# Kernel optimization log

Measured on AMD Instinct MI355X. Metric: run time of the kernel, lower is better.

## Reference

```python
import jax, jax.numpy as jnp
import numpy as np

D_MODEL = 1024
N_HEADS = 16
HEAD = D_MODEL // N_HEADS  # 64


def setup_inputs() -> dict:
    key = jax.random.key(0)
    ks = jax.random.split(key, 9)
    s = 1.0 / np.sqrt(D_MODEL)
    x = jax.random.normal(ks[0], (2, 2048, D_MODEL), dtype=jnp.float32)
    Wq = jax.random.uniform(ks[1], (N_HEADS, D_MODEL, HEAD), jnp.float32, -s, s)
    bq = jax.random.uniform(ks[2], (N_HEADS, HEAD), jnp.float32, -s, s)
    Wk = jax.random.uniform(ks[3], (N_HEADS, D_MODEL, HEAD), jnp.float32, -s, s)
    bk = jax.random.uniform(ks[4], (N_HEADS, HEAD), jnp.float32, -s, s)
    Wv = jax.random.uniform(ks[5], (N_HEADS, D_MODEL, HEAD), jnp.float32, -s, s)
    bv = jax.random.uniform(ks[6], (N_HEADS, HEAD), jnp.float32, -s, s)
    Wo = jax.random.uniform(ks[7], (D_MODEL, D_MODEL), jnp.float32, -s, s)
    bo = jax.random.uniform(ks[8], (D_MODEL,), jnp.float32, -s, s)
    return {"x": x, "Wq": Wq, "bq": bq, "Wk": Wk, "bk": bk,
            "Wv": Wv, "bv": bv, "Wo": Wo, "bo": bo}


def reference(x, Wq, bq, Wk, bk, Wv, bv, Wo, bo):
    # Per-head projections, vectorized over heads: [B,S,D] x [H,D,h] -> [B,H,S,h]
    Q = jnp.einsum('bsd,hdk->bhsk', x, Wq) + bq[None, :, None, :]
    K = jnp.einsum('bsd,hdk->bhsk', x, Wk) + bk[None, :, None, :]
    V = jnp.einsum('bsd,hdk->bhsk', x, Wv) + bv[None, :, None, :]
    scores = jnp.einsum('bhqk,bhsk->bhqs', Q, K) / jnp.sqrt(jnp.float32(HEAD))
    attn = jax.nn.softmax(scores, axis=-1)  # dropout is identity in eval mode
    out = jnp.einsum('bhqs,bhsk->bhqk', attn, V)  # [B,H,S,h]
    B, H, S, h = out.shape
    out = out.transpose(0, 2, 1, 3).reshape(B, S, H * h)  # concat heads -> [B,S,D]
    return out @ Wo.T + bo if False else jnp.einsum('bsd,ed->bse', out, Wo.T.T) + bo
```

## Files before the change

kernel.cpp:

```cpp
#include <hip/hip_runtime.h>
#include <hip/hip_bf16.h>

typedef unsigned short u16;
typedef short short8 __attribute__((ext_vector_type(8)));
typedef float floatx4 __attribute__((ext_vector_type(4)));

#define MFMA16(a, b, c) __builtin_amdgcn_mfma_f32_16x16x32_bf16((a), (b), (c), 0, 0, 0)

union U64u { unsigned long long ll; u16 s[4]; };
union U128u { uint4 q; u16 s[8]; };

__device__ __forceinline__ u16 f2bf(float f) {
  union { float f; unsigned u; } v; v.f = f;
  unsigned r = v.u + 0x7fffu + ((v.u >> 16) & 1u);
  return (u16)(r >> 16);
}

__device__ __forceinline__ void async16(const u16* g, u16* l) {
  __builtin_amdgcn_global_load_lds(
      (const __attribute__((address_space(1))) unsigned int*)g,
      (__attribute__((address_space(3))) unsigned int*)l, 16, 0, 0);
}


__global__ __launch_bounds__(256) void cast_f2b(const float* __restrict__ src,
                                                u16* __restrict__ dst, int n4) {
  int i = blockIdx.x * 256 + threadIdx.x;
  if (i >= n4) return;
  float4 v = ((const float4*)src)[i];
  U64u o;
  o.s[0] = f2bf(v.x); o.s[1] = f2bf(v.y); o.s[2] = f2bf(v.z); o.s[3] = f2bf(v.w);
  ((unsigned long long*)dst)[i] = o.ll;
}

__global__ __launch_bounds__(256) void prep_wqkv(
    const float* __restrict__ Wq, const float* __restrict__ bq,
    const float* __restrict__ Wk, const float* __restrict__ bk,
    const float* __restrict__ Wv, const float* __restrict__ bv,
    u16* __restrict__ Wt, float* __restrict__ ball) {
  int id = blockIdx.x * 256 + threadIdx.x;
  int kk4 = id & 15;
  int d = (id >> 4) & 1023;
  int h = (id >> 14) & 15;
  int wsel = id >> 18;
  const float* W = wsel == 0 ? Wq : (wsel == 1 ? Wk : Wv);
  float4 v = *(const float4*)(W + ((size_t)(h * 1024 + d)) * 64 + kk4 * 4);
  int nb = wsel * 1024 + h * 64 + kk4 * 4;
  Wt[(size_t)(nb + 0) * 1024 + d] = f2bf(v.x);
  Wt[(size_t)(nb + 1) * 1024 + d] = f2bf(v.y);
  Wt[(size_t)(nb + 2) * 1024 + d] = f2bf(v.z);
  Wt[(size_t)(nb + 3) * 1024 + d] = f2bf(v.w);
  if (id < 3072) {
    int ws2 = id >> 10, hk = id & 1023;
    const float* bsrc = ws2 == 0 ? bq : (ws2 == 1 ? bk : bv);
    ball[id] = bsrc[hk];
  }
}

__global__ __launch_bounds__(256) void transpose_v(const u16* __restrict__ QKV,
                                                   u16* __restrict__ Vt) {
  __shared__ u16 t[64][65];
  int tid = threadIdx.x;
  int bh = blockIdx.y, b = bh >> 4, h = bh & 15;
  int s0 = blockIdx.x * 64;
  {
    int r = tid >> 2, c0 = (tid & 3) * 16;
    const u16* src = QKV + (size_t)(b * 2048 + s0 + r) * 3072 + 2048 + h * 64 + c0;
    U128u a, c;
    a.q = *(const uint4*)src;
    c.q = *(const uint4*)(src + 8);
#pragma unroll
    for (int j = 0; j < 8; ++j) { t[r][c0 + j] = a.s[j]; t[r][c0 + 8 + j] = c.s[j]; }
  }
  __syncthreads();
  {
    int dl = tid >> 2, sp = (tid & 3) * 16;
    U128u oa, ob;
#pragma unroll
    for (int j = 0; j < 8; ++j) { oa.s[j] = t[sp + j][dl]; ob.s[j] = t[sp + 8 + j][dl]; }
    u16* dst = Vt + (size_t)(bh * 64 + dl) * 2048 + s0 + sp;
    *(uint4*)dst = oa.q;
    *(uint4*)(dst + 8) = ob.q;
  }
}


__device__ __forceinline__ void store_out(u16* p, float v) { *p = f2bf(v); }
__device__ __forceinline__ void store_out(float* p, float v) { *p = v; }

template <typename OutT>
__global__ __launch_bounds__(256) void gemm_bt(
    const u16* __restrict__ A, const u16* __restrict__ B,
    const float* __restrict__ bias, OutT* __restrict__ C,
    int M, int N, int K, int scaleNend, float scaleVal) {
  __shared__ __attribute__((aligned(16))) u16 As[128 * 32];
  __shared__ __attribute__((aligned(16))) u16 Bs[128 * 32];
  const int tid = threadIdx.x;
  const int w = tid >> 6, lane = tid & 63;
  const int l15 = lane & 15, l4 = lane >> 4;
  const int bm = blockIdx.y, bn = blockIdx.x;
  const int wm = (w & 1) * 64, wn = (w >> 1) * 64;

  floatx4 acc[4][4];
#pragma unroll
  for (int i = 0; i < 4; ++i)
#pragma unroll
    for (int j = 0; j < 4; ++j) acc[i][j] = (floatx4){0.f, 0.f, 0.f, 0.f};

  for (int k0 = 0; k0 < K; k0 += 32) {
    __syncthreads();
#pragma unroll
    for (int j = 0; j < 2; ++j) {
      int c = j * 4 + w;
      int row = c * 16 + (lane >> 2);
      int ko = (lane & 3) * 8;
      async16(A + (size_t)(bm * 128 + row) * K + k0 + ko, As + c * 512);
      async16(B + (size_t)(bn * 128 + row) * K + k0 + ko, Bs + c * 512);
    }
    __syncthreads();
    short8 af[4], bf[4];
#pragma unroll
    for (int t = 0; t < 4; ++t) {
      af[t] = *(const short8*)(As + (wm + t * 16 + l15) * 32 + l4 * 8);
      bf[t] = *(const short8*)(Bs + (wn + t * 16 + l15) * 32 + l4 * 8);
    }
#pragma unroll
    for (int tm = 0; tm < 4; ++tm)
#pragma unroll
      for (int tn = 0; tn < 4; ++tn) acc[tm][tn] = MFMA16(af[tm], bf[tn], acc[tm][tn]);
  }

#pragma unroll
  for (int tn = 0; tn < 4; ++tn) {
    int col = bn * 128 + wn + tn * 16 + l15;
    float bv = bias[col];
    float sc = (col < scaleNend) ? scaleVal : 1.0f;
#pragma unroll
    for (int tm = 0; tm < 4; ++tm) {
      int row0 = bm * 128 + wm + tm * 16 + l4 * 4;
#pragma unroll
      for (int r = 0; r < 4; ++r) {
        float v = (acc[tm][tn][r] + bv) * sc;
        store_out(C + (size_t)(row0 + r) * N + col, v);
      }
    }
  }
}


__global__ __launch_bounds__(256) void attn_kernel(const u16* __restrict__ QKV,
                                                   const u16* __restrict__ Vt,
                                                   u16* __restrict__ O) {
  __shared__ __attribute__((aligned(16))) u16 Ks[128 * 64];
  __shared__ __attribute__((aligned(16))) u16 Vs[64 * 128];
  __shared__ __attribute__((aligned(16))) u16 Ps[128 * 136];

  const int tid = threadIdx.x;
  const int w = tid >> 6, lane = tid & 63;
  const int l15 = lane & 15, l4 = lane >> 4;
  const int q0 = blockIdx.x * 128;
  const int bh = blockIdx.y;
  const int b = bh >> 4, h = bh & 15;

  short8 qf[2][2];
  {
    const u16* Qb = QKV + (size_t)(b * 2048 + q0 + w * 32) * 3072 + h * 64;
#pragma unroll
    for (int tq = 0; tq < 2; ++tq)
#pragma unroll
      for (int kc = 0; kc < 2; ++kc)
        qf[tq][kc] = *(const short8*)(Qb + (size_t)(tq * 16 + l15) * 3072 + kc * 32 + l4 * 8);
  }

  floatx4 Oacc[2][4];
#pragma unroll
  for (int i = 0; i < 2; ++i)
#pragma unroll
    for (int j = 0; j < 4; ++j) Oacc[i][j] = (floatx4){0.f, 0.f, 0.f, 0.f};
  float lpart[2] = {0.f, 0.f};

  const u16* Kb = QKV + (size_t)(b * 2048) * 3072 + 1024 + h * 64;
  const u16* Vb = Vt + (size_t)bh * 64 * 2048;

  for (int kt = 0; kt < 16; ++kt) {
    __syncthreads();
#pragma unroll
    for (int j = 0; j < 4; ++j) {
      int c = j * 4 + w;
      {
        int row = c * 8 + (lane >> 3);
        int gch = (lane & 7) ^ ((lane >> 3) & 7);
        async16(Kb + (size_t)(kt * 128 + row) * 3072 + gch * 8, Ks + c * 512);
      }
      {
        int d = c * 4 + l4;
        int gch = l15 ^ (d & 15);
        async16(Vb + (size_t)d * 2048 + kt * 128 + gch * 8, Vs + c * 512);
      }
    }
    __syncthreads();

#pragma unroll
    for (int tk = 0; tk < 8; ++tk) {
      int krow = tk * 16 + l15;
      int sw = krow & 7;
      short8 kf0 = *(const short8*)(Ks + krow * 64 + ((l4) ^ sw) * 8);
      short8 kf1 = *(const short8*)(Ks + krow * 64 + ((4 + l4) ^ sw) * 8);
#pragma unroll
      for (int tq = 0; tq < 2; ++tq) {
        floatx4 s = (floatx4){0.f, 0.f, 0.f, 0.f};
        s = MFMA16(kf0, qf[tq][0], s);
        s = MFMA16(kf1, qf[tq][1], s);
        U64u pk;
#pragma unroll
        for (int r = 0; r < 4; ++r) {
          float p = __expf(s[r]);
          lpart[tq] += p;
          pk.s[r] = f2bf(p);
        }
        *(unsigned long long*)(Ps + (size_t)(w * 32 + tq * 16 + l15) * 136 + tk * 16 + l4 * 4) = pk.ll;
      }
    }

    short8 pf[2][4];
#pragma unroll
    for (int tq = 0; tq < 2; ++tq)
#pragma unroll
      for (int kc = 0; kc < 4; ++kc)
        pf[tq][kc] = *(const short8*)(Ps + (size_t)(w * 32 + tq * 16 + l15) * 136 + kc * 32 + l4 * 8);
#pragma unroll
    for (int td = 0; td < 4; ++td)
#pragma unroll
      for (int kc = 0; kc < 4; ++kc) {
        int drow = td * 16 + l15;
        short8 vf = *(const short8*)(Vs + drow * 128 + (((kc << 2) | l4) ^ l15) * 8);
#pragma unroll
        for (int tq = 0; tq < 2; ++tq) Oacc[tq][td] = MFMA16(pf[tq][kc], vf, Oacc[tq][td]);
      }
  }

  float linv[2];
#pragma unroll
  for (int tq = 0; tq < 2; ++tq) {
    float l = lpart[tq];
    l += __shfl_xor(l, 16);
    l += __shfl_xor(l, 32);
    linv[tq] = 1.0f / l;
  }
  float iv[2][4];
#pragma unroll
  for (int tq = 0; tq < 2; ++tq)
#pragma unroll
    for (int r = 0; r < 4; ++r) iv[tq][r] = __shfl(linv[tq], l4 * 4 + r);

  u16* Ob = O + (size_t)(b * 2048 + q0 + w * 32) * 1024 + h * 64;
#pragma unroll
  for (int tq = 0; tq < 2; ++tq)
#pragma unroll
    for (int td = 0; td < 4; ++td)
#pragma unroll
      for (int r = 0; r < 4; ++r)
        Ob[(size_t)(tq * 16 + l4 * 4 + r) * 1024 + td * 16 + l15] =
            f2bf(Oacc[tq][td][r] * iv[tq][r]);
}


extern "C" void kernel_launch(void* const* d_in, const int* in_sizes, int n_in,
                              void* d_out, int out_size, void* d_ws, size_t ws_size,
                              hipStream_t stream) {
  const float* x  = (const float*)d_in[0];
  const float* Wq = (const float*)d_in[1];
  const float* bq = (const float*)d_in[2];
  const float* Wk = (const float*)d_in[3];
  const float* bk = (const float*)d_in[4];
  const float* Wv = (const float*)d_in[5];
  const float* bv = (const float*)d_in[6];
  const float* Wo = (const float*)d_in[7];
  const float* bo = (const float*)d_in[8];

  char* p = (char*)d_ws;
  u16* Xb   = (u16*)p; p += (size_t)4096 * 1024 * 2;
  u16* Wt   = (u16*)p; p += (size_t)3072 * 1024 * 2;
  u16* QKV  = (u16*)p; p += (size_t)4096 * 3072 * 2;
  u16* Vtp  = (u16*)p; p += (size_t)2 * 16 * 64 * 2048 * 2;
  u16* Ob   = (u16*)p; p += (size_t)4096 * 1024 * 2;
  u16* Wob  = (u16*)p; p += (size_t)1024 * 1024 * 2;
  float* ball = (float*)p; p += 3072 * sizeof(float);

  cast_f2b<<<4096, 256, 0, stream>>>(x, Xb, 1048576);
  cast_f2b<<<1024, 256, 0, stream>>>(Wo, Wob, 262144);
  prep_wqkv<<<3072, 256, 0, stream>>>(Wq, bq, Wk, bk, Wv, bv, Wt, ball);
  gemm_bt<u16><<<dim3(24, 32), 256, 0, stream>>>(Xb, Wt, ball, QKV,
                                                 4096, 3072, 1024, 1024, 0.125f);
  transpose_v<<<dim3(32, 32), 256, 0, stream>>>(QKV, Vtp);
  attn_kernel<<<dim3(16, 32), 256, 0, stream>>>(QKV, Vtp, Ob);
  gemm_bt<float><<<dim3(8, 32), 256, 0, stream>>>(Ob, Wob, bo, (float*)d_out,
                                                  4096, 1024, 1024, 0, 1.0f);
}
```

Before: 227.6 us.

## Split attention keys across waves with per-wave LDS and LDS reduction

The attention kernel now processes 64 queries per block, and each wave handles a disjoint quarter of the key range with its own LDS buffers. This removes block-wide barriers in the main loop in favour of per-wave waitcnt, and the waves' partial outputs and row sums are merged with LDS atomics at the end. The softmax uses exp2 with log2(e) folded into the Q scale, and bf16 packing uses a perm instruction. The output-projection GEMM uses 64-wide N tiles to launch more blocks. The cost is an LDS atomic reduction at the end, and the rounding in pk2 differs from round-to-nearest-even.

```diff
diff --git a/kernel.cpp b/kernel.cpp
--- a/kernel.cpp
+++ b/kernel.cpp
@@ -7,13 +7,26 @@
 
 #define MFMA16(a, b, c) __builtin_amdgcn_mfma_f32_16x16x32_bf16((a), (b), (c), 0, 0, 0)
 
-union U64u { unsigned long long ll; u16 s[4]; };
 union U128u { uint4 q; u16 s[8]; };
 
 __device__ __forceinline__ u16 f2bf(float f) {
   union { float f; unsigned u; } v; v.f = f;
   unsigned r = v.u + 0x7fffu + ((v.u >> 16) & 1u);
   return (u16)(r >> 16);
+}
+
+__device__ __forceinline__ unsigned pk2(float hi, float lo) {
+  union { float f; unsigned u; } a, b;
+  a.f = hi; b.f = lo;
+  return __builtin_amdgcn_perm(a.u + 0x8000u, b.u + 0x8000u, 0x07060302u);
+}
+
+__device__ __forceinline__ float fexp2(float x) {
+#if __has_builtin(__builtin_amdgcn_exp2f)
+  return __builtin_amdgcn_exp2f(x);
+#else
+  return exp2f(x);
+#endif
 }
 
 __device__ __forceinline__ void async16(const u16* g, u16* l) {
@@ -28,7 +41,7 @@
   int i = blockIdx.x * 256 + threadIdx.x;
   if (i >= n4) return;
   float4 v = ((const float4*)src)[i];
-  U64u o;
+  union { unsigned long long ll; u16 s[4]; } o;
   o.s[0] = f2bf(v.x); o.s[1] = f2bf(v.y); o.s[2] = f2bf(v.z); o.s[3] = f2bf(v.w);
   ((unsigned long long*)dst)[i] = o.ll;
 }
@@ -88,51 +101,57 @@
 __device__ __forceinline__ void store_out(u16* p, float v) { *p = f2bf(v); }
 __device__ __forceinline__ void store_out(float* p, float v) { *p = v; }
 
-template <typename OutT>
+template <int BN, typename OutT>
 __global__ __launch_bounds__(256) void gemm_bt(
     const u16* __restrict__ A, const u16* __restrict__ B,
     const float* __restrict__ bias, OutT* __restrict__ C,
     int M, int N, int K, int scaleNend, float scaleVal) {
+  constexpr int TN = BN / 32;
   __shared__ __attribute__((aligned(16))) u16 As[128 * 32];
-  __shared__ __attribute__((aligned(16))) u16 Bs[128 * 32];
+  __shared__ __attribute__((aligned(16))) u16 Bs[BN * 32];
   const int tid = threadIdx.x;
   const int w = tid >> 6, lane = tid & 63;
   const int l15 = lane & 15, l4 = lane >> 4;
   const int bm = blockIdx.y, bn = blockIdx.x;
-  const int wm = (w & 1) * 64, wn = (w >> 1) * 64;
-
-  floatx4 acc[4][4];
+  const int wm = (w & 1) * 64, wn = (w >> 1) * (BN / 2);
+
+  floatx4 acc[4][TN];
 #pragma unroll
   for (int i = 0; i < 4; ++i)
 #pragma unroll
-    for (int j = 0; j < 4; ++j) acc[i][j] = (floatx4){0.f, 0.f, 0.f, 0.f};
+    for (int j = 0; j < TN; ++j) acc[i][j] = (floatx4){0.f, 0.f, 0.f, 0.f};
 
   for (int k0 = 0; k0 < K; k0 += 32) {
     __syncthreads();
 #pragma unroll
     for (int j = 0; j < 2; ++j) {
-      int c = j * 4 + w;
-      int row = c * 16 + (lane >> 2);
-      int ko = (lane & 3) * 8;
-      async16(A + (size_t)(bm * 128 + row) * K + k0 + ko, As + c * 512);
-      async16(B + (size_t)(bn * 128 + row) * K + k0 + ko, Bs + c * 512);
+      int i = j * 256 + tid;
+      int row = i >> 2, ko = (i & 3) * 8;
+      async16(A + (size_t)(bm * 128 + row) * K + k0 + ko, As + (j * 256 + w * 64) * 8);
+    }
+#pragma unroll
+    for (int j = 0; j < BN / 64; ++j) {
+      int i = j * 256 + tid;
+      int row = i >> 2, ko = (i & 3) * 8;
+      async16(B + (size_t)(bn * BN + row) * K + k0 + ko, Bs + (j * 256 + w * 64) * 8);
     }
     __syncthreads();
-    short8 af[4], bf[4];
-#pragma unroll
-    for (int t = 0; t < 4; ++t) {
+    short8 af[4], bf[TN];
+#pragma unroll
+    for (int t = 0; t < 4; ++t)
       af[t] = *(const short8*)(As + (wm + t * 16 + l15) * 32 + l4 * 8);
+#pragma unroll
+    for (int t = 0; t < TN; ++t)
       bf[t] = *(const short8*)(Bs + (wn + t * 16 + l15) * 32 + l4 * 8);
-    }
 #pragma unroll
     for (int tm = 0; tm < 4; ++tm)
 #pragma unroll
-      for (int tn = 0; tn < 4; ++tn) acc[tm][tn] = MFMA16(af[tm], bf[tn], acc[tm][tn]);
-  }
-
-#pragma unroll
-  for (int tn = 0; tn < 4; ++tn) {
-    int col = bn * 128 + wn + tn * 16 + l15;
+      for (int tn = 0; tn < TN; ++tn) acc[tm][tn] = MFMA16(af[tm], bf[tn], acc[tm][tn]);
+  }
+
+#pragma unroll
+  for (int tn = 0; tn < TN; ++tn) {
+    int col = bn * BN + wn + tn * 16 + l15;
     float bv = bias[col];
     float sc = (col < scaleNend) ? scaleVal : 1.0f;
 #pragma unroll
@@ -148,120 +167,130 @@
 }
 
 
-__global__ __launch_bounds__(256) void attn_kernel(const u16* __restrict__ QKV,
-                                                   const u16* __restrict__ Vt,
-                                                   u16* __restrict__ O) {
-  __shared__ __attribute__((aligned(16))) u16 Ks[128 * 64];
-  __shared__ __attribute__((aligned(16))) u16 Vs[64 * 128];
-  __shared__ __attribute__((aligned(16))) u16 Ps[128 * 136];
-
+__global__ __launch_bounds__(256, 3) void attn_kernel(const u16* __restrict__ QKV,
+                                                      const u16* __restrict__ Vt,
+                                                      u16* __restrict__ O) {
+  __shared__ __attribute__((aligned(16))) u16 lds[26624];
   const int tid = threadIdx.x;
   const int w = tid >> 6, lane = tid & 63;
   const int l15 = lane & 15, l4 = lane >> 4;
-  const int q0 = blockIdx.x * 128;
-  const int bh = blockIdx.y;
-  const int b = bh >> 4, h = bh & 15;
-
-  short8 qf[2][2];
+  const int q0 = blockIdx.x * 64;
+  const int bh = blockIdx.y, b = bh >> 4, h = bh & 15;
+
+  u16* Ksw = lds + w * 2048;
+  u16* Vsw = lds + 8192 + w * 2048;
+  u16* Psw = lds + 16384 + w * 2560;
+
+  short8 qf[4][2];
   {
-    const u16* Qb = QKV + (size_t)(b * 2048 + q0 + w * 32) * 3072 + h * 64;
-#pragma unroll
-    for (int tq = 0; tq < 2; ++tq)
-#pragma unroll
-      for (int kc = 0; kc < 2; ++kc)
-        qf[tq][kc] = *(const short8*)(Qb + (size_t)(tq * 16 + l15) * 3072 + kc * 32 + l4 * 8);
-  }
-
-  floatx4 Oacc[2][4];
-#pragma unroll
-  for (int i = 0; i < 2; ++i)
+    const u16* Qb = QKV + (size_t)(b * 2048 + q0) * 3072 + h * 64;
+#pragma unroll
+    for (int tq = 0; tq < 4; ++tq)
+#pragma unroll
+      for (int s = 0; s < 2; ++s)
+        qf[tq][s] = *(const short8*)(Qb + (size_t)(tq * 16 + l15) * 3072 + s * 32 + l4 * 8);
+  }
+
+  floatx4 Oacc[4][4];
+#pragma unroll
+  for (int i = 0; i < 4; ++i)
 #pragma unroll
     for (int j = 0; j < 4; ++j) Oacc[i][j] = (floatx4){0.f, 0.f, 0.f, 0.f};
-  float lpart[2] = {0.f, 0.f};
+  float lpart[4] = {0.f, 0.f, 0.f, 0.f};
 
   const u16* Kb = QKV + (size_t)(b * 2048) * 3072 + 1024 + h * 64;
   const u16* Vb = Vt + (size_t)bh * 64 * 2048;
 
-  for (int kt = 0; kt < 16; ++kt) {
-    __syncthreads();
-#pragma unroll
-    for (int j = 0; j < 4; ++j) {
-      int c = j * 4 + w;
-      {
-        int row = c * 8 + (lane >> 3);
-        int gch = (lane & 7) ^ ((lane >> 3) & 7);
-        async16(Kb + (size_t)(kt * 128 + row) * 3072 + gch * 8, Ks + c * 512);
-      }
-      {
-        int d = c * 4 + l4;
-        int gch = l15 ^ (d & 15);
-        async16(Vb + (size_t)d * 2048 + kt * 128 + gch * 8, Vs + c * 512);
-      }
-    }
-    __syncthreads();
-
-#pragma unroll
-    for (int tk = 0; tk < 8; ++tk) {
+  for (int it = 0; it < 16; ++it) {
+    const int key0 = w * 512 + it * 32;
+    __builtin_amdgcn_s_waitcnt(0xC07F);
+#pragma unroll
+    for (int r = 0; r < 4; ++r) {
+      int i = r * 64 + lane;
+      int k = i >> 3, c = i & 7;
+      async16(Kb + (size_t)(key0 + k) * 3072 + (c ^ (k & 7)) * 8, Ksw + r * 512);
+    }
+#pragma unroll
+    for (int r = 0; r < 4; ++r) {
+      int i = r * 64 + lane;
+      int d = i >> 2, c = i & 3;
+      int sw = (d ^ (d >> 2)) & 3;
+      async16(Vb + (size_t)d * 2048 + key0 + (c ^ sw) * 8, Vsw + r * 512);
+    }
+    __builtin_amdgcn_s_waitcnt(0x0F70);
+
+#pragma unroll
+    for (int tk = 0; tk < 2; ++tk) {
       int krow = tk * 16 + l15;
-      int sw = krow & 7;
-      short8 kf0 = *(const short8*)(Ks + krow * 64 + ((l4) ^ sw) * 8);
-      short8 kf1 = *(const short8*)(Ks + krow * 64 + ((4 + l4) ^ sw) * 8);
-#pragma unroll
-      for (int tq = 0; tq < 2; ++tq) {
+      int swk = l15 & 7;
+      short8 kf0 = *(const short8*)(Ksw + krow * 64 + (l4 ^ swk) * 8);
+      short8 kf1 = *(const short8*)(Ksw + krow * 64 + ((4 + l4) ^ swk) * 8);
+#pragma unroll
+      for (int tq = 0; tq < 4; ++tq) {
         floatx4 s = (floatx4){0.f, 0.f, 0.f, 0.f};
         s = MFMA16(kf0, qf[tq][0], s);
         s = MFMA16(kf1, qf[tq][1], s);
-        U64u pk;
-#pragma unroll
-        for (int r = 0; r < 4; ++r) {
-          float p = __expf(s[r]);
-          lpart[tq] += p;
-          pk.s[r] = f2bf(p);
-        }
-        *(unsigned long long*)(Ps + (size_t)(w * 32 + tq * 16 + l15) * 136 + tk * 16 + l4 * 4) = pk.ll;
+        float p0 = fexp2(s[0]), p1 = fexp2(s[1]), p2 = fexp2(s[2]), p3 = fexp2(s[3]);
+        lpart[tq] += (p0 + p1) + (p2 + p3);
+        unsigned lo = pk2(p1, p0), hi = pk2(p3, p2);
+        *(unsigned long long*)(Psw + (size_t)(tq * 16 + l15) * 40 + tk * 16 + l4 * 4) =
+            ((unsigned long long)hi << 32) | lo;
       }
     }
 
-    short8 pf[2][4];
-#pragma unroll
-    for (int tq = 0; tq < 2; ++tq)
-#pragma unroll
-      for (int kc = 0; kc < 4; ++kc)
-        pf[tq][kc] = *(const short8*)(Ps + (size_t)(w * 32 + tq * 16 + l15) * 136 + kc * 32 + l4 * 8);
-#pragma unroll
-    for (int td = 0; td < 4; ++td)
-#pragma unroll
-      for (int kc = 0; kc < 4; ++kc) {
-        int drow = td * 16 + l15;
-        short8 vf = *(const short8*)(Vs + drow * 128 + (((kc << 2) | l4) ^ l15) * 8);
-#pragma unroll
-        for (int tq = 0; tq < 2; ++tq) Oacc[tq][td] = MFMA16(pf[tq][kc], vf, Oacc[tq][td]);
-      }
-  }
-
-  float linv[2];
-#pragma unroll
-  for (int tq = 0; tq < 2; ++tq) {
+    short8 pf[4];
+#pragma unroll
+    for (int tq = 0; tq < 4; ++tq)
+      pf[tq] = *(const short8*)(Psw + (size_t)(tq * 16 + l15) * 40 + l4 * 8);
+#pragma unroll
+    for (int td = 0; td < 4; ++td) {
+      int d = td * 16 + l15;
+      int sw = (d ^ (d >> 2)) & 3;
+      short8 vf = *(const short8*)(Vsw + d * 32 + (l4 ^ sw) * 8);
+#pragma unroll
+      for (int tq = 0; tq < 4; ++tq) Oacc[tq][td] = MFMA16(pf[tq], vf, Oacc[tq][td]);
+    }
+  }
+
+  float lr[4];
+#pragma unroll
+  for (int tq = 0; tq < 4; ++tq) {
     float l = lpart[tq];
     l += __shfl_xor(l, 16);
     l += __shfl_xor(l, 32);
-    linv[tq] = 1.0f / l;
-  }
-  float iv[2][4];
-#pragma unroll
-  for (int tq = 0; tq < 2; ++tq)
-#pragma unroll
-    for (int r = 0; r < 4; ++r) iv[tq][r] = __shfl(linv[tq], l4 * 4 + r);
-
-  u16* Ob = O + (size_t)(b * 2048 + q0 + w * 32) * 1024 + h * 64;
-#pragma unroll
-  for (int tq = 0; tq < 2; ++tq)
+    lr[tq] = l;
+  }
+
+  __syncthreads();
+  float* fb = (float*)lds;
+  float* lsh = fb + 64 * 68;
+  for (int i = tid; i < 64 * 68 + 64; i += 256) fb[i] = 0.f;
+  __syncthreads();
+#pragma unroll
+  for (int tq = 0; tq < 4; ++tq)
 #pragma unroll
     for (int td = 0; td < 4; ++td)
 #pragma unroll
       for (int r = 0; r < 4; ++r)
-        Ob[(size_t)(tq * 16 + l4 * 4 + r) * 1024 + td * 16 + l15] =
-            f2bf(Oacc[tq][td][r] * iv[tq][r]);
+        atomicAdd(&fb[(size_t)(tq * 16 + l4 * 4 + r) * 68 + td * 16 + l15], Oacc[tq][td][r]);
+  if (l4 == 0) {
+#pragma unroll
+    for (int tq = 0; tq < 4; ++tq) atomicAdd(&lsh[tq * 16 + l15], lr[tq]);
+  }
+  __syncthreads();
+
+  {
+    int row = tid >> 2, c0 = (tid & 3) * 16;
+    float inv = 1.0f / lsh[row];
+    U128u o1, o2;
+#pragma unroll
+    for (int j = 0; j < 8; ++j) o1.s[j] = f2bf(fb[(size_t)row * 68 + c0 + j] * inv);
+#pragma unroll
+    for (int j = 0; j < 8; ++j) o2.s[j] = f2bf(fb[(size_t)row * 68 + c0 + 8 + j] * inv);
+    u16* Op = O + (size_t)(b * 2048 + q0 + row) * 1024 + h * 64 + c0;
+    *(uint4*)Op = o1.q;
+    *(uint4*)(Op + 8) = o2.q;
+  }
 }
 
 
@@ -287,13 +316,15 @@
   u16* Wob  = (u16*)p; p += (size_t)1024 * 1024 * 2;
   float* ball = (float*)p; p += 3072 * sizeof(float);
 
+  const float qscale = 0.125f * 1.4426950408889634f;
+
   cast_f2b<<<4096, 256, 0, stream>>>(x, Xb, 1048576);
   cast_f2b<<<1024, 256, 0, stream>>>(Wo, Wob, 262144);
   prep_wqkv<<<3072, 256, 0, stream>>>(Wq, bq, Wk, bk, Wv, bv, Wt, ball);
-  gemm_bt<u16><<<dim3(24, 32), 256, 0, stream>>>(Xb, Wt, ball, QKV,
-                                                 4096, 3072, 1024, 1024, 0.125f);
+  gemm_bt<128, u16><<<dim3(24, 32), 256, 0, stream>>>(Xb, Wt, ball, QKV,
+                                                      4096, 3072, 1024, 1024, qscale);
   transpose_v<<<dim3(32, 32), 256, 0, stream>>>(QKV, Vtp);
-  attn_kernel<<<dim3(16, 32), 256, 0, stream>>>(QKV, Vtp, Ob);
-  gemm_bt<float><<<dim3(8, 32), 256, 0, stream>>>(Ob, Wob, bo, (float*)d_out,
-                                                  4096, 1024, 1024, 0, 1.0f);
-}
+  attn_kernel<<<dim3(32, 32), 256, 0, stream>>>(QKV, Vtp, Ob);
+  gemm_bt<64, float><<<dim3(16, 32), 256, 0, stream>>>(Ob, Wob, bo, (float*)d_out,
+                                                       4096, 1024, 1024, 0, 1.0f);
+}
```

New measurement: 298.8 us. +31.3%, slower.
